# Kernel tuning notes

Hardware: AMD Instinct MI355X
Metric: run time of the kernel (lower is better)

The kernel has to match this reference:

```python
import jax, jax.numpy as jnp
import numpy as np

LAM = 0.1   # smooth_param
EPS = 1e-8  # torch cosine_similarity eps


def setup_inputs() -> dict:
    key = jax.random.key(0)
    k1, k2, k3 = jax.random.split(key, 3)
    B, num_supp, num_query, T, D = 8, 5, 128, 16, 2048
    supp = jax.random.normal(k1, (B, num_supp, T, D), jnp.float32)
    query = jax.random.normal(k2, (B, num_query, T, D), jnp.float32)
    query_ys = jax.random.randint(k3, (B * num_query,), 0, num_supp)
    return {"supp": supp, "query": query, "query_ys": query_ys}


def _cosine_dist(supp, query):
    # supp: (B, ns, T, D), query: (B, nq, T, D)
    # dist[b,q,s,l,m] = 1 - cos(supp[b,s,l], query[b,q,m]); batch order (b,q,s)
    B, ns, T, D = supp.shape
    nq = query.shape[1]
    dots = jnp.einsum('bsld,bqmd->bqslm', supp, query)
    sn = jnp.linalg.norm(supp, axis=-1)   # (B, ns, T)
    qn = jnp.linalg.norm(query, axis=-1)  # (B, nq, T)
    denom = jnp.maximum(sn[:, None, :, :, None] * qn[:, :, None, None, :], EPS)
    dist = 1.0 - dots / denom
    return dist.reshape(B * nq * ns, T, T)


def _dtw(dist):
    # Relaxed (soft-min) OTAM band DP. dist: (N, T, T) -> (N,)
    # opt grid is (T, T+2) with zero-padded columns m=0 and m=T+1.
    N, T, _ = dist.shape
    dist_pad = jnp.pad(dist, ((0, 0), (0, 0), (1, 1)))  # (N, T, T+2)
    # Row l=0: opt[0,m] = cumsum of dist_pad[0, :m+1]
    row0 = jnp.cumsum(dist_pad[:, 0, :], axis=-1)  # (N, T+2)

    m_idx = jnp.arange(1, T + 2)
    boundary = (m_idx == 1) | (m_idx == T + 1)  # 3-way softmin only at band edges

    def row_step(prev_row, dist_row):
        # prev_row: (N, T+2) = opt[l-1]; dist_row: (N, T+2) = dist_pad[:, l]
        def col_step(left, xs):
            diag, up, d, is_b = xs  # each (N,) except is_b scalar bool
            s2 = jnp.logaddexp(-diag / LAM, -left / LAM)        # {diag, left}
            s3 = jnp.logaddexp(s2, -up / LAM)                   # + {up}
            val = -LAM * jnp.where(is_b, s3, s2) + d
            return val, val

        xs = (prev_row[:, :-1].T, prev_row[:, 1:].T, dist_row[:, 1:].T, boundary)
        init = jnp.zeros((N,), dist_row.dtype)  # opt[l, 0] = 0
        _, cols = jax.lax.scan(col_step, init, xs)  # (T+1, N)
        new_row = jnp.concatenate([init[:, None], cols.T], axis=1)  # (N, T+2)
        return new_row, None

    rows = jnp.swapaxes(dist_pad[:, 1:, :], 0, 1)  # (T-1, N, T+2)
    final_row, _ = jax.lax.scan(row_step, row0, rows)
    return final_row[:, -1]  # opt[:, T-1, T+1]


def _cross_entropy(logits, labels):
    logp = jax.nn.log_softmax(logits, axis=-1)
    return -jnp.mean(jnp.take_along_axis(logp, labels[:, None], axis=1))


def reference(supp, query, query_ys):
    ns = supp.shape[1]
    dist = _cosine_dist(supp, query)            # (B*nq*ns, T, T)
    tam1 = _dtw(dist).reshape(-1, ns)           # forward-direction alignment
    tam2 = _dtw(dist[:, ::-1, ::-1]).reshape(-1, ns)  # flipped (dims 1,2)
    loss1 = _cross_entropy(-tam1, query_ys)
    loss2 = _cross_entropy(-tam2, query_ys)
    loss = 0.5 * (loss1 + loss2)
    tam = 0.5 * (tam1 + tam2)
    return loss, tam
```

## Files before the change

kernel.cpp:

```cpp
#include <hip/hip_runtime.h>
#include <hip/hip_bf16.h>

#define NB   8
#define NS   5
#define NQ   128
#define TT   16
#define DD   2048
#define BK   64
#define LDK  72
#define NROW 1024
#define NTH  384
#define LAMI 10.0f
#define LAMF 0.1f

typedef __attribute__((ext_vector_type(8))) short  short8;
typedef __attribute__((ext_vector_type(4))) float  float4v;

static __device__ __forceinline__ unsigned int f2bf2(float x, float y) {
    union { float f; unsigned int u; } a, b; a.f = x; b.f = y;
    unsigned int ra = a.u + 0x7fffu + ((a.u >> 16) & 1u);
    unsigned int rb = b.u + 0x7fffu + ((b.u >> 16) & 1u);
    return (ra >> 16) | (rb & 0xffff0000u);
}

static __device__ __forceinline__ float lse2(float x, float y) {
    float mx = fmaxf(x, y), mn = fminf(x, y);
    return mx + __logf(1.0f + __expf(mn - mx));
}

__global__ __launch_bounds__(NTH, 6) void
dist_dtw_kernel(const float* __restrict__ supp, const float* __restrict__ query,
                float* __restrict__ out_tam, float* __restrict__ t1w, float* __restrict__ t2w)
{
    __shared__ __align__(16) unsigned short sAB[2][96 * LDK];
    __shared__ float ssq[96];
    __shared__ float distS[NS][TT][TT];
    __shared__ float tamv[16];

    const int tid  = threadIdx.x;
    const int blk  = blockIdx.x;
    const int wave = tid >> 6;
    const int lane = tid & 63;
    const int fr   = lane & 15;
    const int quad = lane >> 4;

    const float* qbase = query + (size_t)blk * (TT * DD);
    const float* sbase = supp  + (size_t)(blk >> 7) * (NS * TT * DD);

    const float* gp[4];
    int lo[4];
    int rowj[4];
    #pragma unroll
    for (int j = 0; j < 4; ++j) {
        int idx = j * NTH + tid;
        int row = idx >> 4;
        int col = idx & 15;
        rowj[j] = row;
        gp[j] = (row < 80 ? sbase + (size_t)row * DD
                          : qbase + (size_t)(row - 80) * DD) + col * 4;
        lo[j] = row * LDK + col * 4;
    }

    float4 regs[2][4];
    #pragma unroll
    for (int j = 0; j < 4; ++j) regs[0][j] = *reinterpret_cast<const float4*>(gp[j]);

    float ss[4] = {0.f, 0.f, 0.f, 0.f};
    float4v acc = {0.f, 0.f, 0.f, 0.f};

    #pragma unroll 2
    for (int k = 0; k < DD / BK; ++k) {
        const int buf = k & 1;
        if (k < DD / BK - 1) {
            #pragma unroll
            for (int j = 0; j < 4; ++j)
                regs[buf ^ 1][j] = *reinterpret_cast<const float4*>(gp[j] + (k + 1) * BK);
        }
        #pragma unroll
        for (int j = 0; j < 4; ++j) {
            float4 v = regs[buf][j];
            uint2 pv = { f2bf2(v.x, v.y), f2bf2(v.z, v.w) };
            *reinterpret_cast<uint2*>(&sAB[buf][lo[j]]) = pv;
            ss[j] += v.x * v.x + v.y * v.y + v.z * v.z + v.w * v.w;
        }
        __syncthreads();
        if (wave < NS) {
            const unsigned short* arow = &sAB[buf][(wave * 16 + fr) * LDK];
            const unsigned short* brow = &sAB[buf][(80 + fr) * LDK];
            short8 a0 = *reinterpret_cast<const short8*>(arow + quad * 8);
            short8 b0 = *reinterpret_cast<const short8*>(brow + quad * 8);
            acc = __builtin_amdgcn_mfma_f32_16x16x32_bf16(a0, b0, acc, 0, 0, 0);
            short8 a1 = *reinterpret_cast<const short8*>(arow + 32 + quad * 8);
            short8 b1 = *reinterpret_cast<const short8*>(brow + 32 + quad * 8);
            acc = __builtin_amdgcn_mfma_f32_16x16x32_bf16(a1, b1, acc, 0, 0, 0);
        }
    }

    #pragma unroll
    for (int j = 0; j < 4; ++j) {
        float v = ss[j];
        v += __shfl_xor(v, 1, 16);
        v += __shfl_xor(v, 2, 16);
        v += __shfl_xor(v, 4, 16);
        v += __shfl_xor(v, 8, 16);
        if ((tid & 15) == 0) ssq[rowj[j]] = v;
    }
    __syncthreads();

    if (wave < NS) {
        float qn = sqrtf(ssq[80 + fr]);
        #pragma unroll
        for (int r = 0; r < 4; ++r) {
            int l = quad * 4 + r;
            float denom = fmaxf(sqrtf(ssq[wave * 16 + l]) * qn, 1e-8f);
            distS[wave][l][fr] = 1.0f - acc[r] / denom;
        }
    }
    __syncthreads();

    if (wave < NS && (lane & 31) <= 17) {
        const int g   = lane & 31;
        const int dir = lane >> 5;
        const int s   = wave;
        float val = 0.f, vprev = 0.f;
        #pragma unroll
        for (int t = 1; t <= 32; ++t) {
            float left = __shfl_up(val,   1, 32);
            float diag = __shfl_up(vprev, 1, 32);
            int l = t - g;
            if (g >= 1 && l >= 0 && l <= 15) {
                float d = 0.f;
                if (g <= 16) d = dir ? distS[s][15 - l][16 - g] : distS[s][l][g - 1];
                float nv;
                if (l == 0) {
                    nv = left + d;
                } else if (g == 1 || g == 17) {
                    nv = -LAMF * lse2(lse2(-diag * LAMI, -left * LAMI), -val * LAMI) + d;
                } else {
                    float lo2 = fminf(diag, left), hi2 = fmaxf(diag, left);
                    nv = lo2 - LAMF * __logf(1.0f + __expf((lo2 - hi2) * LAMI)) + d;
                }
                vprev = val; val = nv;
            }
        }
        if (g == 17) tamv[s * 2 + dir] = val;
    }
    __syncthreads();

    if (tid < NS) {
        float t1 = tamv[2 * tid], t2 = tamv[2 * tid + 1];
        int n = blk * NS + tid;
        t1w[n] = t1;
        t2w[n] = t2;
        out_tam[n] = 0.5f * (t1 + t2);
    }
}

__global__ __launch_bounds__(1024) void
loss_kernel(const float* __restrict__ t1w, const float* __restrict__ t2w,
            const int* __restrict__ ys, float* __restrict__ out)
{
    __shared__ float red[16];
    const int row = threadIdx.x;

    float t1[NS], t2[NS];
    #pragma unroll
    for (int s = 0; s < NS; ++s) { t1[s] = t1w[row * NS + s]; t2[s] = t2w[row * NS + s]; }
    const int y = ys[row];

    float mx1 = -t1[0], mx2 = -t2[0];
    #pragma unroll
    for (int s = 1; s < NS; ++s) { mx1 = fmaxf(mx1, -t1[s]); mx2 = fmaxf(mx2, -t2[s]); }
    float s1 = 0.f, s2 = 0.f;
    #pragma unroll
    for (int s = 0; s < NS; ++s) { s1 += __expf(-t1[s] - mx1); s2 += __expf(-t2[s] - mx2); }
    float lse1  = mx1 + __logf(s1);
    float lse2v = mx2 + __logf(s2);

    float ty1 = t1[0], ty2 = t2[0];
    #pragma unroll
    for (int s = 1; s < NS; ++s) { if (y == s) { ty1 = t1[s]; ty2 = t2[s]; } }

    float c = 0.5f * ((lse1 + ty1) + (lse2v + ty2));

    #pragma unroll
    for (int off = 32; off >= 1; off >>= 1) c += __shfl_down(c, off, 64);
    if ((row & 63) == 0) red[row >> 6] = c;
    __syncthreads();
    if (row == 0) {
        float tot = 0.f;
        #pragma unroll
        for (int i = 0; i < 16; ++i) tot += red[i];
        out[0] = tot * (1.0f / (float)NROW);
    }
}

extern "C" void kernel_launch(void* const* d_in, const int* in_sizes, int n_in,
                              void* d_out, int out_size, void* d_ws, size_t ws_size,
                              hipStream_t stream) {
    const float* supp  = (const float*)d_in[0];
    const float* query = (const float*)d_in[1];
    const int*   ys    = (const int*)d_in[2];
    float* out = (float*)d_out;

    float* t1w = (float*)d_ws;
    float* t2w = t1w + NROW * NS;

    dist_dtw_kernel<<<NROW, NTH, 0, stream>>>(supp, query, out + 1, t1w, t2w);
    loss_kernel<<<1, 1024, 0, stream>>>(t1w, t2w, ys, out);
}
```

Measured before the change: 256.4 us.

## Precompute bf16 copies and row norms in a separate pass, stream MFMA operands from global

A new preprocessing kernel converts supp and query to bf16 once and computes each row's sum of squares. The distance/DTW kernel then loads bf16 MFMA operands straight from global memory, with no LDS staging and no per-tile __syncthreads, using 5 waves and two independent accumulators. The aim is to stop every block re-reading and re-converting the fp32 support set, and to halve the bytes the main kernel reads. The cost is an extra full pass that writes and re-reads a bf16 copy of query, plus one more kernel launch.

```diff
diff --git a/kernel.cpp b/kernel.cpp
--- a/kernel.cpp
+++ b/kernel.cpp
@@ -6,10 +6,10 @@
 #define NQ   128
 #define TT   16
 #define DD   2048
-#define BK   64
-#define LDK  72
 #define NROW 1024
-#define NTH  384
+#define NSROW (NB * NS * TT)
+#define NQROW (NROW * TT)
+#define NRTOT (NSROW + NQROW)
 #define LAMI 10.0f
 #define LAMF 0.1f
 
@@ -23,16 +23,47 @@
     return (ra >> 16) | (rb & 0xffff0000u);
 }
 
-static __device__ __forceinline__ float lse2(float x, float y) {
+static __device__ __forceinline__ float lse2f(float x, float y) {
     float mx = fmaxf(x, y), mn = fminf(x, y);
     return mx + __logf(1.0f + __expf(mn - mx));
 }
 
-__global__ __launch_bounds__(NTH, 6) void
-dist_dtw_kernel(const float* __restrict__ supp, const float* __restrict__ query,
+__global__ __launch_bounds__(256) void
+preproc_kernel(const float* __restrict__ supp, const float* __restrict__ query,
+               unsigned short* __restrict__ suppBf, unsigned short* __restrict__ queryBf,
+               float* __restrict__ suppSq, float* __restrict__ querySq)
+{
+    const int wave = threadIdx.x >> 6, lane = threadIdx.x & 63;
+    const int row = blockIdx.x * 4 + wave;
+    const float* src; unsigned short* dst; float* sqp;
+    if (row < NSROW) {
+        src = supp + (size_t)row * DD;  dst = suppBf + (size_t)row * DD;  sqp = suppSq + row;
+    } else {
+        int r = row - NSROW;
+        src = query + (size_t)r * DD;   dst = queryBf + (size_t)r * DD;   sqp = querySq + r;
+    }
+    float ss = 0.f;
+    #pragma unroll
+    for (int i = 0; i < 8; ++i) {
+        float4 v = *reinterpret_cast<const float4*>(src + i * 256 + lane * 4);
+        uint2 pv = { f2bf2(v.x, v.y), f2bf2(v.z, v.w) };
+        *reinterpret_cast<uint2*>(dst + i * 256 + lane * 4) = pv;
+        ss += v.x * v.x + v.y * v.y + v.z * v.z + v.w * v.w;
+    }
+    ss += __shfl_xor(ss, 32, 64);
+    ss += __shfl_xor(ss, 16, 64);
+    ss += __shfl_xor(ss, 8, 64);
+    ss += __shfl_xor(ss, 4, 64);
+    ss += __shfl_xor(ss, 2, 64);
+    ss += __shfl_xor(ss, 1, 64);
+    if (lane == 0) *sqp = ss;
+}
+
+__global__ __launch_bounds__(320) void
+dist_dtw_kernel(const unsigned short* __restrict__ suppBf, const unsigned short* __restrict__ queryBf,
+                const float* __restrict__ suppSq, const float* __restrict__ querySq,
                 float* __restrict__ out_tam, float* __restrict__ t1w, float* __restrict__ t2w)
 {
-    __shared__ __align__(16) unsigned short sAB[2][96 * LDK];
     __shared__ float ssq[96];
     __shared__ float distS[NS][TT][TT];
     __shared__ float tamv[16];
@@ -44,81 +75,38 @@
     const int fr   = lane & 15;
     const int quad = lane >> 4;
 
-    const float* qbase = query + (size_t)blk * (TT * DD);
-    const float* sbase = supp  + (size_t)(blk >> 7) * (NS * TT * DD);
-
-    const float* gp[4];
-    int lo[4];
-    int rowj[4];
-    #pragma unroll
-    for (int j = 0; j < 4; ++j) {
-        int idx = j * NTH + tid;
-        int row = idx >> 4;
-        int col = idx & 15;
-        rowj[j] = row;
-        gp[j] = (row < 80 ? sbase + (size_t)row * DD
-                          : qbase + (size_t)(row - 80) * DD) + col * 4;
-        lo[j] = row * LDK + col * 4;
-    }
-
-    float4 regs[2][4];
-    #pragma unroll
-    for (int j = 0; j < 4; ++j) regs[0][j] = *reinterpret_cast<const float4*>(gp[j]);
-
-    float ss[4] = {0.f, 0.f, 0.f, 0.f};
-    float4v acc = {0.f, 0.f, 0.f, 0.f};
-
-    #pragma unroll 2
-    for (int k = 0; k < DD / BK; ++k) {
-        const int buf = k & 1;
-        if (k < DD / BK - 1) {
-            #pragma unroll
-            for (int j = 0; j < 4; ++j)
-                regs[buf ^ 1][j] = *reinterpret_cast<const float4*>(gp[j] + (k + 1) * BK);
-        }
-        #pragma unroll
-        for (int j = 0; j < 4; ++j) {
-            float4 v = regs[buf][j];
-            uint2 pv = { f2bf2(v.x, v.y), f2bf2(v.z, v.w) };
-            *reinterpret_cast<uint2*>(&sAB[buf][lo[j]]) = pv;
-            ss[j] += v.x * v.x + v.y * v.y + v.z * v.z + v.w * v.w;
-        }
-        __syncthreads();
-        if (wave < NS) {
-            const unsigned short* arow = &sAB[buf][(wave * 16 + fr) * LDK];
-            const unsigned short* brow = &sAB[buf][(80 + fr) * LDK];
-            short8 a0 = *reinterpret_cast<const short8*>(arow + quad * 8);
-            short8 b0 = *reinterpret_cast<const short8*>(brow + quad * 8);
-            acc = __builtin_amdgcn_mfma_f32_16x16x32_bf16(a0, b0, acc, 0, 0, 0);
-            short8 a1 = *reinterpret_cast<const short8*>(arow + 32 + quad * 8);
-            short8 b1 = *reinterpret_cast<const short8*>(brow + 32 + quad * 8);
-            acc = __builtin_amdgcn_mfma_f32_16x16x32_bf16(a1, b1, acc, 0, 0, 0);
-        }
-    }
-
-    #pragma unroll
-    for (int j = 0; j < 4; ++j) {
-        float v = ss[j];
-        v += __shfl_xor(v, 1, 16);
-        v += __shfl_xor(v, 2, 16);
-        v += __shfl_xor(v, 4, 16);
-        v += __shfl_xor(v, 8, 16);
-        if ((tid & 15) == 0) ssq[rowj[j]] = v;
-    }
-    __syncthreads();
-
-    if (wave < NS) {
+    if (tid < 80)      ssq[tid] = suppSq[(blk >> 7) * (NS * TT) + tid];
+    else if (tid < 96) ssq[tid] = querySq[blk * TT + (tid - 80)];
+
+    const unsigned short* ap =
+        suppBf + ((size_t)((blk >> 7) * NS + wave) * TT + fr) * DD + quad * 8;
+    const unsigned short* bp =
+        queryBf + ((size_t)blk * TT + fr) * DD + quad * 8;
+
+    float4v acc0 = {0.f, 0.f, 0.f, 0.f}, acc1 = {0.f, 0.f, 0.f, 0.f};
+    #pragma unroll 8
+    for (int k = 0; k < 64; k += 2) {
+        short8 a0 = *reinterpret_cast<const short8*>(ap + k * 32);
+        short8 b0 = *reinterpret_cast<const short8*>(bp + k * 32);
+        short8 a1 = *reinterpret_cast<const short8*>(ap + k * 32 + 32);
+        short8 b1 = *reinterpret_cast<const short8*>(bp + k * 32 + 32);
+        acc0 = __builtin_amdgcn_mfma_f32_16x16x32_bf16(a0, b0, acc0, 0, 0, 0);
+        acc1 = __builtin_amdgcn_mfma_f32_16x16x32_bf16(a1, b1, acc1, 0, 0, 0);
+    }
+    __syncthreads();
+
+    {
         float qn = sqrtf(ssq[80 + fr]);
         #pragma unroll
         for (int r = 0; r < 4; ++r) {
             int l = quad * 4 + r;
             float denom = fmaxf(sqrtf(ssq[wave * 16 + l]) * qn, 1e-8f);
-            distS[wave][l][fr] = 1.0f - acc[r] / denom;
+            distS[wave][l][fr] = 1.0f - (acc0[r] + acc1[r]) / denom;
         }
     }
     __syncthreads();
 
-    if (wave < NS && (lane & 31) <= 17) {
+    if ((lane & 31) <= 17) {
         const int g   = lane & 31;
         const int dir = lane >> 5;
         const int s   = wave;
@@ -135,7 +123,7 @@
                 if (l == 0) {
                     nv = left + d;
                 } else if (g == 1 || g == 17) {
-                    nv = -LAMF * lse2(lse2(-diag * LAMI, -left * LAMI), -val * LAMI) + d;
+                    nv = -LAMF * lse2f(lse2f(-diag * LAMI, -left * LAMI), -val * LAMI) + d;
                 } else {
                     float lo2 = fminf(diag, left), hi2 = fmaxf(diag, left);
                     nv = lo2 - LAMF * __logf(1.0f + __expf((lo2 - hi2) * LAMI)) + d;
@@ -203,9 +191,14 @@
     const int*   ys    = (const int*)d_in[2];
     float* out = (float*)d_out;
 
-    float* t1w = (float*)d_ws;
-    float* t2w = t1w + NROW * NS;
-
-    dist_dtw_kernel<<<NROW, NTH, 0, stream>>>(supp, query, out + 1, t1w, t2w);
+    float* t1w     = (float*)d_ws;
+    float* t2w     = t1w + NROW * NS;
+    float* suppSq  = t2w + NROW * NS;
+    float* querySq = suppSq + NSROW;
+    unsigned short* suppBf  = (unsigned short*)(querySq + NQROW);
+    unsigned short* queryBf = suppBf + (size_t)NSROW * DD;
+
+    preproc_kernel<<<NRTOT / 4, 256, 0, stream>>>(supp, query, suppBf, queryBf, suppSq, querySq);
+    dist_dtw_kernel<<<NROW, 320, 0, stream>>>(suppBf, queryBf, suppSq, querySq, out + 1, t1w, t2w);
     loss_kernel<<<1, 1024, 0, stream>>>(t1w, t2w, ys, out);
 }
```

Measured after the change: 291.4 us. 1.14x slower.
